# Optimization experiments

Hardware: AMD Instinct MI355X
Metric: run time of the kernel (lower is better)

The kernel has to match this reference:

```python
import jax, jax.numpy as jnp
import numpy as np

D_MODEL = 768
D_STATE = 128
D_CONV = 4
EXPAND = 4
D_INNER = EXPAND * D_MODEL  # 3072
DT_RANK = 48  # ceil(768/16), mamba default dt_rank='auto'
H_MLP = 768
EPS = 1e-6


def setup_inputs() -> dict:
    key = jax.random.key(0)
    ks = jax.random.split(key, 12)
    B, T = 1, 384

    def rn(k, shape, s=0.02):
        return jax.random.normal(k, shape, jnp.float32) * s

    inp = {}
    inp["x"] = jax.random.normal(ks[0], (B, 3 * T, D_MODEL), jnp.float32)
    inp["ln_w"] = jnp.ones((6, D_MODEL), jnp.float32)  # ln1..ln6 RMSNorm weights
    # 3 independent Mamba blocks, params stacked on leading dim
    inp["in_proj_w"] = rn(ks[1], (3, 2 * D_INNER, D_MODEL))
    inp["conv_w"] = rn(ks[2], (3, D_INNER, 1, D_CONV), 0.1)  # depthwise causal conv1d
    inp["conv_b"] = rn(ks[3], (3, D_INNER), 0.1)
    inp["x_proj_w"] = rn(ks[4], (3, DT_RANK + 2 * D_STATE, D_INNER))
    inp["dt_proj_w"] = rn(ks[5], (3, D_INNER, DT_RANK), 0.1)
    inp["dt_proj_b"] = rn(ks[6], (3, D_INNER), 0.1) - 4.0  # small dt after softplus
    A = jnp.tile(jnp.arange(1, D_STATE + 1, dtype=jnp.float32)[None, None, :], (3, D_INNER, 1))
    inp["A_log"] = jnp.log(A)  # mamba S4D-real init
    inp["D_skip"] = jnp.ones((3, D_INNER), jnp.float32)
    inp["out_proj_w"] = rn(ks[7], (3, D_MODEL, D_INNER))
    # 3 GatedMLPs: fc1 -> 2*hidden (value, gate), silu gate, fc2 -> out
    inp["fc1_w"] = rn(ks[8], (3, 2 * H_MLP, D_MODEL))
    inp["fc1_b"] = jnp.zeros((3, 2 * H_MLP), jnp.float32)
    inp["fc2_w"] = rn(ks[9], (3, D_MODEL, H_MLP))
    inp["fc2_b"] = jnp.zeros((3, D_MODEL), jnp.float32)
    return inp


def _rmsnorm(x, w):
    v = jnp.mean(jnp.square(x), axis=-1, keepdims=True)
    return x * jax.lax.rsqrt(v + EPS) * w


def _mamba(u, in_w, cw, cb, xp_w, dt_w, dt_b, A_log, D_skip, out_w):
    # u: (B, T, D_MODEL)
    Bsz = u.shape[0]
    xz = u @ in_w.T  # (B,T,2*Di)
    x, z = jnp.split(xz, 2, axis=-1)
    # causal depthwise conv1d over time
    xc = jax.lax.conv_general_dilated(
        jnp.swapaxes(x, 1, 2), cw, (1,), [(D_CONV - 1, 0)],
        feature_group_count=D_INNER)  # (B,Di,T)
    x = jax.nn.silu(jnp.swapaxes(xc, 1, 2) + cb)  # (B,T,Di)
    x_dbl = x @ xp_w.T  # (B,T,dt_rank+2N)
    dt = x_dbl[..., :DT_RANK]
    Bm = x_dbl[..., DT_RANK:DT_RANK + D_STATE]
    Cm = x_dbl[..., DT_RANK + D_STATE:]
    delta = jax.nn.softplus(dt @ dt_w.T + dt_b)  # (B,T,Di)
    A = -jnp.exp(A_log)  # (Di,N)

    def step(h, inp):
        d_t, B_t, C_t, u_t = inp  # (B,Di),(B,N),(B,N),(B,Di)
        h = jnp.exp(d_t[:, :, None] * A) * h + (d_t * u_t)[:, :, None] * B_t[:, None, :]
        y = jnp.einsum('bdn,bn->bd', h, C_t)
        return h, y

    h0 = jnp.zeros((Bsz, D_INNER, D_STATE), u.dtype)
    xs = tuple(jnp.swapaxes(a, 0, 1) for a in (delta, Bm, Cm, x))  # time-major
    _, ys = jax.lax.scan(jax.checkpoint(step), h0, xs)
    y = jnp.swapaxes(ys, 0, 1) + x * D_skip  # (B,T,Di)
    return (y * jax.nn.silu(z)) @ out_w.T  # (B,T,D_MODEL)


def _gmlp(x, w1, b1, w2, b2):
    h = x @ w1.T + b1
    a, g = jnp.split(h, 2, axis=-1)
    return (jax.nn.silu(g) * a) @ w2.T + b2


def reference(x, ln_w, in_proj_w, conv_w, conv_b, x_proj_w, dt_proj_w, dt_proj_b,
              A_log, D_skip, out_proj_w, fc1_w, fc1_b, fc2_w, fc2_b):
    t = x.shape[1] // 3
    outs = []
    for i in range(3):  # music / up / down branches
        b = x[:, i * t:(i + 1) * t]
        b = b + _mamba(_rmsnorm(b, ln_w[2 * i]), in_proj_w[i], conv_w[i], conv_b[i],
                       x_proj_w[i], dt_proj_w[i], dt_proj_b[i], A_log[i], D_skip[i],
                       out_proj_w[i])
        b = b + _gmlp(_rmsnorm(b, ln_w[2 * i + 1]), fc1_w[i], fc1_b[i], fc2_w[i], fc2_b[i])
        outs.append(b)
    return jnp.concatenate(outs, axis=1)
```

## Files before the change

kernel.cpp:

```cpp
#include <hip/hip_runtime.h>
#include <hip/hip_bf16.h>

#define TSEQ 384
#define DMODEL 768
#define DINNER 3072
#define DSTATE 128
#define DTRANK 48
#define XPROJ_N (DTRANK + 2*DSTATE)
#define NSEG 3
#define LOG2E 1.44269504088896340736f
#define LN2F  0.69314718055994530942f

typedef __attribute__((ext_vector_type(8))) short short8;
typedef __attribute__((ext_vector_type(4))) float floatx4;
typedef unsigned short u16;
typedef unsigned int u32;

__device__ __forceinline__ float bf2f(u16 u) {
    return __uint_as_float(((unsigned)u) << 16);
}
__device__ __forceinline__ float ldf(const void* p, size_t i, int bf) {
    return bf ? bf2f(((const u16*)p)[i]) : ((const float*)p)[i];
}
__device__ __forceinline__ void stf(void* p, size_t i, float v, int bf) {
    if (bf) ((__hip_bfloat16*)p)[i] = __float2bfloat16(v);
    else    ((float*)p)[i] = v;
}
__device__ __forceinline__ float silu_f(float v) { return v / (1.f + __expf(-v)); }
__device__ __forceinline__ u16 f2bf(float f) {
    unsigned u = __float_as_uint(f);
    return (u16)((u + 0x7FFFu + ((u >> 16) & 1u)) >> 16);
}

__device__ __forceinline__ float exp2_fast(float x) {
#if __has_builtin(__builtin_amdgcn_exp2f)
    return __builtin_amdgcn_exp2f(x);
#else
    return exp2f(x);
#endif
}

template<int CTRL>
__device__ __forceinline__ float ror_add(float x) {
    int r = __builtin_amdgcn_update_dpp(0, __float_as_int(x), CTRL, 0xF, 0xF, true);
    return x + __int_as_float(r);
}

__device__ __forceinline__ void gl16(const void* g, void* l) {
    __builtin_amdgcn_global_load_lds(
        (const __attribute__((address_space(1))) u32*)g,
        (__attribute__((address_space(3))) u32*)l, 16, 0, 0);
}

__global__ void k_detect(const unsigned* lnw_bits, int* flag) {
    if (threadIdx.x == 0) {
        flag[0] = (lnw_bits[0] == 0x3F803F80u) ? 1 : 0;
    }
}

__global__ __launch_bounds__(256) void k_rmsnorm(
    const void* src, int src_is_f32, const void* lnw, int wbase,
    u16* out, const int* flagp)
{
    int bf  = *flagp;
    int sbf = src_is_f32 ? 0 : bf;
    int r   = blockIdx.x;
    int seg = r / TSEQ;
    int wrow = 2*seg + wbase;
    int tid = threadIdx.x;
    float v[3]; float s = 0.f;
    #pragma unroll
    for (int j = 0; j < 3; ++j) {
        int e = j*256 + tid;
        v[j] = ldf(src, (size_t)r*DMODEL + e, sbf);
        s += v[j]*v[j];
    }
    __shared__ float red[256];
    red[tid] = s; __syncthreads();
    for (int st = 128; st > 0; st >>= 1) {
        if (tid < st) red[tid] += red[tid+st];
        __syncthreads();
    }
    float rs = rsqrtf(red[0]/(float)DMODEL + 1e-6f);
    #pragma unroll
    for (int j = 0; j < 3; ++j) {
        int e = j*256 + tid;
        out[(size_t)r*DMODEL + e] = f2bf(v[j]*rs*ldf(lnw, (size_t)wrow*DMODEL + e, bf));
    }
}

__global__ __launch_bounds__(256) void k_gemm(
    const float* A, const void* W, const void* bias,
    float* C, const int* flagp, int M, int N, int K, int lda)
{
    int bf  = *flagp;
    int seg = blockIdx.z;
    int mbase = blockIdx.y * 64, nbase = blockIdx.x * 64;
    int tid = threadIdx.x;
    int tx = tid & 15, ty = tid >> 4;

    __shared__ float As[16][68];
    __shared__ float Ws[16][68];

    const float* Ag = A + (size_t)seg*M*lda;
    size_t segW = (size_t)seg*N*K;

    int lrow = tid >> 2;
    int lk   = (tid & 3) * 4;
    int wn   = nbase + lrow;

    float acc[4][4];
    #pragma unroll
    for (int i = 0; i < 4; ++i)
        #pragma unroll
        for (int j = 0; j < 4; ++j) acc[i][j] = 0.f;

    for (int kt = 0; kt < K; kt += 16) {
        float4 av = *reinterpret_cast<const float4*>(Ag + (size_t)(mbase+lrow)*lda + kt + lk);
        As[lk+0][lrow] = av.x; As[lk+1][lrow] = av.y;
        As[lk+2][lrow] = av.z; As[lk+3][lrow] = av.w;
        float w0=0.f, w1=0.f, w2=0.f, w3=0.f;
        if (wn < N) {
            size_t off = segW + (size_t)wn*K + kt + lk;
            if (bf) {
                ushort4 q = *reinterpret_cast<const ushort4*>((const u16*)W + off);
                w0 = bf2f(q.x); w1 = bf2f(q.y); w2 = bf2f(q.z); w3 = bf2f(q.w);
            } else {
                float4 f = *reinterpret_cast<const float4*>((const float*)W + off);
                w0 = f.x; w1 = f.y; w2 = f.z; w3 = f.w;
            }
        }
        Ws[lk+0][lrow] = w0; Ws[lk+1][lrow] = w1;
        Ws[lk+2][lrow] = w2; Ws[lk+3][lrow] = w3;
        __syncthreads();
        #pragma unroll
        for (int kk = 0; kk < 16; ++kk) {
            float4 a4 = *reinterpret_cast<const float4*>(&As[kk][ty*4]);
            float4 b4 = *reinterpret_cast<const float4*>(&Ws[kk][tx*4]);
            float ar[4] = {a4.x, a4.y, a4.z, a4.w};
            float br[4] = {b4.x, b4.y, b4.z, b4.w};
            #pragma unroll
            for (int i = 0; i < 4; ++i)
                #pragma unroll
                for (int j = 0; j < 4; ++j)
                    acc[i][j] = fmaf(ar[i], br[j], acc[i][j]);
        }
        __syncthreads();
    }

    #pragma unroll
    for (int i = 0; i < 4; ++i) {
        int m = mbase + ty*4 + i;
        #pragma unroll
        for (int j = 0; j < 4; ++j) {
            int n = nbase + tx*4 + j;
            if (n < N) {
                float v = acc[i][j] + ldf(bias, (size_t)seg*N + n, bf);
                v = (v > 20.f) ? v : log1pf(__expf(v));
                C[((size_t)(seg*M + m))*N + n] = v;
            }
        }
    }
}

__global__ __launch_bounds__(256) void k_gemm_mfma64g(
    const u16* A, const void* W, const void* bias, const void* resid,
    int resid_flagged, void* C, int c_mode, const int* flagp,
    int M, int N, int K)
{
    int bf  = *flagp;
    int seg = blockIdx.z;
    int mbase = blockIdx.y * 64, nbase = blockIdx.x * 64;
    int tid = threadIdx.x;
    int w = tid >> 6, lane = tid & 63;
    int wm = w >> 1, wn = w & 1;
    int quad = lane >> 4, l16 = lane & 15;

    __shared__ short As[3][64*64];
    __shared__ short Ws[3][64*64];

    const u16* Ag = A + (size_t)seg*M*K + (size_t)mbase*K;
    size_t segWK = (size_t)seg*N*K;
    int nk = K >> 6;

    int srow = lane >> 3;
    int scol = ((lane & 7) ^ srow) * 8;
    int swz  = (l16 & 7) * 8;

    floatx4 acc[2][2];
    #pragma unroll
    for (int i = 0; i < 2; ++i)
        #pragma unroll
        for (int j = 0; j < 2; ++j)
            acc[i][j] = (floatx4){0.f, 0.f, 0.f, 0.f};

    auto CMP = [&](int b) {
        #pragma unroll
        for (int kk = 0; kk < 2; ++kk) {
            short8 af[2], bfr[2];
            #pragma unroll
            for (int i = 0; i < 2; ++i) {
                int row = wm*32 + i*16 + l16;
                af[i] = *reinterpret_cast<const short8*>(
                    &As[b][row*64 + (((kk*4 + quad)*8) ^ swz)]);
            }
            #pragma unroll
            for (int j = 0; j < 2; ++j) {
                int row = wn*32 + j*16 + l16;
                bfr[j] = *reinterpret_cast<const short8*>(
                    &Ws[b][row*64 + (((kk*4 + quad)*8) ^ swz)]);
            }
            #pragma unroll
            for (int i = 0; i < 2; ++i)
                #pragma unroll
                for (int j = 0; j < 2; ++j)
                    acc[i][j] = __builtin_amdgcn_mfma_f32_16x16x32_bf16(af[i], bfr[j], acc[i][j], 0, 0, 0);
        }
    };

    if (bf) {
        const u16* Wb = (const u16*)W;
        auto STG = [&](int t, int b) {
            size_t kt = (size_t)t << 6;
            #pragma unroll
            for (int i8 = 0; i8 < 2; ++i8) {
                int rbase = w*16 + i8*8;
                gl16(Ag + (size_t)(rbase + srow)*K + kt + scol, &As[b][rbase*64]);
                int wr = nbase + rbase + srow;
                if (wr > N - 1) wr = N - 1;
                gl16(Wb + segWK + (size_t)wr*K + kt + scol, &Ws[b][rbase*64]);
            }
        };
        STG(0, 0);
        STG(1, 1);
        for (int t = 0; t < nk - 2; ++t) {
            STG(t + 2, (t + 2) % 3);
            asm volatile("s_waitcnt vmcnt(8)" ::: "memory");
            __builtin_amdgcn_s_barrier();
            __builtin_amdgcn_sched_barrier(0);
            CMP(t % 3);
            asm volatile("" ::: "memory");
            __builtin_amdgcn_s_barrier();
        }
        asm volatile("s_waitcnt vmcnt(4)" ::: "memory");
        __builtin_amdgcn_s_barrier();
        __builtin_amdgcn_sched_barrier(0);
        CMP((nk - 2) % 3);
        asm volatile("" ::: "memory");
        __builtin_amdgcn_s_barrier();
        asm volatile("s_waitcnt vmcnt(0)" ::: "memory");
        __builtin_amdgcn_s_barrier();
        __builtin_amdgcn_sched_barrier(0);
        CMP((nk - 1) % 3);
    } else {
        const float* Wf = (const float*)W + segWK;
        int row2 = tid >> 2;
        int wr2 = nbase + row2; if (wr2 > N - 1) wr2 = N - 1;
        for (int t = 0; t < nk; ++t) {
            size_t kt = (size_t)t << 6;
            #pragma unroll
            for (int i8 = 0; i8 < 2; ++i8) {
                int rbase = w*16 + i8*8;
                gl16(Ag + (size_t)(rbase + srow)*K + kt + scol, &As[0][rbase*64]);
            }
            const float* wp = Wf + (size_t)wr2*K + kt;
            #pragma unroll
            for (int h2 = 0; h2 < 2; ++h2) {
                int gs = (tid & 3) + h2*4;
                short8 s;
                #pragma unroll
                for (int q2 = 0; q2 < 8; ++q2) s[q2] = (short)f2bf(wp[gs*8 + q2]);
                *reinterpret_cast<short8*>(&Ws[0][row2*64 + ((gs ^ (row2 & 7)) * 8)]) = s;
            }
            __syncthreads();
            CMP(0);
            __syncthreads();
        }
    }

    #pragma unroll
    for (int i = 0; i < 2; ++i) {
        #pragma unroll
        for (int reg = 0; reg < 4; ++reg) {
            int grow = mbase + wm*32 + i*16 + quad*4 + reg;
            #pragma unroll
            for (int j = 0; j < 2; ++j) {
                int gcol = nbase + wn*32 + j*16 + l16;
                if (gcol < N) {
                    float v = acc[i][j][reg];
                    if (bias) v += ldf(bias, (size_t)seg*N + gcol, bf);
                    size_t idx = ((size_t)(seg*M + grow))*N + gcol;
                    if (resid) v += resid_flagged ? ldf(resid, idx, bf)
                                                  : ((const float*)resid)[idx];
                    if      (c_mode == 0) ((float*)C)[idx] = v;
                    else if (c_mode == 1) ((u16*)C)[idx] = f2bf(v);
                    else                  stf(C, idx, v, bf);
                }
            }
        }
    }
}

__global__ __launch_bounds__(256) void k_fc1_gate_g(
    const u16* A, const void* W, const void* bias, u16* act, const int* flagp)
{
    const int M = TSEQ, K = DMODEL, NF = 2*DMODEL;
    int bf  = *flagp;
    int seg = blockIdx.z;
    int mbase = blockIdx.y * 64, nbase = blockIdx.x * 64;
    int tid = threadIdx.x;
    int w = tid >> 6, lane = tid & 63;
    int wm = w >> 1, wn = w & 1;
    int quad = lane >> 4, l16 = lane & 15;

    __shared__ short As[2][64*64];
    __shared__ short Wa[2][64*64];
    __shared__ short Wg[2][64*64];

    const u16* Ag  = A + (size_t)seg*M*K + (size_t)mbase*K;
    const u16* Wap = (const u16*)W + (size_t)seg*NF*K + (size_t)nbase*K;
    const u16* Wgp = Wap + (size_t)DMODEL*K;
    int nk = K >> 6;

    int srow = lane >> 3;
    int scol = ((lane & 7) ^ srow) * 8;
    int swz  = (l16 & 7) * 8;

    floatx4 acca[2][2], accg[2][2];
    #pragma unroll
    for (int i = 0; i < 2; ++i)
        #pragma unroll
        for (int j = 0; j < 2; ++j) {
            acca[i][j] = (floatx4){0.f, 0.f, 0.f, 0.f};
            accg[i][j] = (floatx4){0.f, 0.f, 0.f, 0.f};
        }

    auto CMP = [&](int b) {
        #pragma unroll
        for (int kk = 0; kk < 2; ++kk) {
            short8 af[2], ba[2], bg[2];
            #pragma unroll
            for (int i = 0; i < 2; ++i) {
                int row = wm*32 + i*16 + l16;
                af[i] = *reinterpret_cast<const short8*>(
                    &As[b][row*64 + (((kk*4 + quad)*8) ^ swz)]);
            }
            #pragma unroll
            for (int j = 0; j < 2; ++j) {
                int row = wn*32 + j*16 + l16;
                int col = ((kk*4 + quad)*8) ^ swz;
                ba[j] = *reinterpret_cast<const short8*>(&Wa[b][row*64 + col]);
                bg[j] = *reinterpret_cast<const short8*>(&Wg[b][row*64 + col]);
            }
            #pragma unroll
            for (int i = 0; i < 2; ++i)
                #pragma unroll
                for (int j = 0; j < 2; ++j) {
                    acca[i][j] = __builtin_amdgcn_mfma_f32_16x16x32_bf16(af[i], ba[j], acca[i][j], 0, 0, 0);
                    accg[i][j] = __builtin_amdgcn_mfma_f32_16x16x32_bf16(af[i], bg[j], accg[i][j], 0, 0, 0);
                }
        }
    };

    if (bf) {
        auto STG = [&](int t, int b) {
            size_t kt = (size_t)t << 6;
            #pragma unroll
            for (int i8 = 0; i8 < 2; ++i8) {
                int rbase = w*16 + i8*8;
                size_t so = (size_t)(rbase + srow)*K + kt + scol;
                gl16(Ag  + so, &As[b][rbase*64]);
                gl16(Wap + so, &Wa[b][rbase*64]);
                gl16(Wgp + so, &Wg[b][rbase*64]);
            }
        };
        STG(0, 0);
        for (int t = 0; t < nk - 1; ++t) {
            STG(t + 1, (t + 1) & 1);
            asm volatile("s_waitcnt vmcnt(6)" ::: "memory");
            __builtin_amdgcn_s_barrier();
            __builtin_amdgcn_sched_barrier(0);
            CMP(t & 1);
            asm volatile("" ::: "memory");
            __builtin_amdgcn_s_barrier();
        }
        asm volatile("s_waitcnt vmcnt(0)" ::: "memory");
        __builtin_amdgcn_s_barrier();
        __builtin_amdgcn_sched_barrier(0);
        CMP((nk - 1) & 1);
    } else {
        const float* Waf = (const float*)W + (size_t)seg*NF*K + (size_t)nbase*K;
        const float* Wgf = Waf + (size_t)DMODEL*K;
        int row2 = tid >> 2;
        for (int t = 0; t < nk; ++t) {
            size_t kt = (size_t)t << 6;
            #pragma unroll
            for (int i8 = 0; i8 < 2; ++i8) {
                int rbase = w*16 + i8*8;
                gl16(Ag + (size_t)(rbase + srow)*K + kt + scol, &As[0][rbase*64]);
            }
            #pragma unroll
            for (int h2 = 0; h2 < 2; ++h2) {
                int gs = (tid & 3) + h2*4;
                int wcol = (gs ^ (row2 & 7)) * 8;
                short8 sa, sg;
                const float* wpa = Waf + (size_t)row2*K + kt + gs*8;
                const float* wpg = Wgf + (size_t)row2*K + kt + gs*8;
                #pragma unroll
                for (int q2 = 0; q2 < 8; ++q2) { sa[q2] = (short)f2bf(wpa[q2]); sg[q2] = (short)f2bf(wpg[q2]); }
                *reinterpret_cast<short8*>(&Wa[0][row2*64 + wcol]) = sa;
                *reinterpret_cast<short8*>(&Wg[0][row2*64 + wcol]) = sg;
            }
            __syncthreads();
            CMP(0);
            __syncthreads();
        }
    }

    #pragma unroll
    for (int i = 0; i < 2; ++i) {
        #pragma unroll
        for (int reg = 0; reg < 4; ++reg) {
            int grow = mbase + wm*32 + i*16 + quad*4 + reg;
            #pragma unroll
            for (int j = 0; j < 2; ++j) {
                int gcol = nbase + wn*32 + j*16 + l16;
                float va = acca[i][j][reg] + ldf(bias, (size_t)seg*NF + gcol, bf);
                float vg = accg[i][j][reg] + ldf(bias, (size_t)seg*NF + DMODEL + gcol, bf);
                act[((size_t)(seg*M + grow))*DMODEL + gcol] = f2bf(va * silu_f(vg));
            }
        }
    }
}

__global__ __launch_bounds__(256) void k_conv(
    const u16* xz, const void* cw, const void* cb, u16* xconv, const int* flagp)
{
    int bf = *flagp;
    size_t gid = (size_t)blockIdx.x*256 + threadIdx.x;
    int d = (int)(gid % DINNER);
    size_t rt = gid / DINNER;
    int t = (int)(rt % TSEQ);
    int seg = (int)(rt / TSEQ);
    float acc = ldf(cb, (size_t)seg*DINNER + d, bf);
    const u16* xs = xz + (size_t)seg*TSEQ*(2*DINNER);
    #pragma unroll
    for (int j = 0; j < 4; ++j) {
        int ts = t - 3 + j;
        if (ts >= 0)
            acc = fmaf(ldf(cw, ((size_t)seg*DINNER + d)*4 + j, bf),
                       bf2f(xs[(size_t)ts*(2*DINNER) + d]), acc);
    }
    xconv[gid] = f2bf(silu_f(acc));
}

#define WSCH 4
#define WSCT 8
#define NPAIR (TSEQ/(2*WSCT))
#define NBX   (DINNER/WSCH)
#define GUARD_TH 0.04f

__global__ __launch_bounds__(64) void k_scan_wave(
    const float* delta, const u16* xconv, const float* xdbl, const u16* xz,
    const void* A_log, const void* D_skip, u16* yout, const int* flagp)
{
    int bf   = flagp[0];
    int seg  = blockIdx.y;
    int bx = (int)blockIdx.x;
    bx = (bx & 7) * (NBX/8) + (bx >> 3);
    int dbase = bx * WSCH;
    int lane = threadIdx.x;
    int ch = lane >> 4, sl = lane & 15;
    int d = dbase + ch;

    __shared__ float4 BUF[2][WSCT][64];
    __shared__ float  DLB2[WSCT][8];

    float a[8];
    size_t abase = ((size_t)seg*DINNER + d)*DSTATE + (size_t)sl*8;
    #pragma unroll
    for (int j = 0; j < 8; ++j)
        a[j] = -__expf(ldf(A_log, abase + j, bf)) * LOG2E;
    float gl[8]; float gmax = 0.f;
    gl[0] = 0.f;
    #pragma unroll
    for (int j = 1; j < 8; ++j) {
        gl[j] = (a[j] - a[j-1]) * LN2F;
        gmax = fmaxf(gmax, fabsf(gl[j]));
    }
    float wg = gmax;
    #pragma unroll
    for (int k = 32; k >= 1; k >>= 1) wg = fmaxf(wg, __shfl_xor(wg, k));
    float a0  = a[0];
    float Dsk = ldf(D_skip, (size_t)seg*DINNER + d, bf);
    float dskg = (sl == 0) ? Dsk : 0.f;

    const float* xdbl_s = xdbl + (size_t)seg*TSEQ*XPROJ_N;
    int loff = DTRANK + (lane & 15)*8 + ((lane >> 4) & 1)*4 + ((lane >> 5) ? DSTATE : 0);
    const float* srcl = xdbl_s + loff;

    const float* delta_s = delta + (size_t)seg*TSEQ*DINNER + dbase;
    const u16*   xconv_s = xconv + (size_t)seg*TSEQ*DINNER + dbase;
    const u16*   z_s     = xz    + (size_t)seg*TSEQ*(2*DINNER) + DINNER + dbase + ch;
    u16*         y_s     = yout  + (size_t)seg*TSEQ*DINNER + dbase + ch;

    float4  pdel = (float4){0.f, 0.f, 0.f, 0.f};
    ushort4 pu   = (ushort4){0, 0, 0, 0};
    u16     pz   = 0;

    auto STAGE = [&](int tile, int buf) {
        const float* rb = srcl + (size_t)tile*WSCT*XPROJ_N;
        #pragma unroll
        for (int t = 0; t < WSCT; ++t)
            gl16(rb + (size_t)t*XPROJ_N, &BUF[buf][t][0]);
    };
    auto PLOAD = [&](int tile) {
        if (lane < WSCT) {
            size_t ro = (size_t)(tile*WSCT + lane)*DINNER;
            pdel = *reinterpret_cast<const float4*>(delta_s + ro);
            pu   = *reinterpret_cast<const ushort4*>(xconv_s + ro);
        }
    };
    auto DSTORE = [&]() -> bool {
        if (lane < WSCT) {
            float4 w0 = (float4){pdel.x, bf2f(pu.x), pdel.y, bf2f(pu.y)};
            float4 w1 = (float4){pdel.z, bf2f(pu.z), pdel.w, bf2f(pu.w)};
            *reinterpret_cast<float4*>(&DLB2[lane][0]) = w0;
            *reinterpret_cast<float4*>(&DLB2[lane][4]) = w1;
        }
        float m4 = fmaxf(fmaxf(pdel.x, pdel.y), fmaxf(pdel.z, pdel.w));
        return __any(m4 * wg > GUARD_TH);
    };

    float h[8];
    #pragma unroll
    for (int j = 0; j < 8; ++j) h[j] = 0.f;
    float yr = 0.f;

    float2 duA, duB, duC;
    float4 b0A, b1A, c0A, c1A;
    float4 b0B, b1B, c0B, c1B;
    float4 b0C, b1C, c0C, c1C;

#define LOADOPS(BP, T, S) do {                                                \
    du##S = *reinterpret_cast<const float2*>(&DLB2[T][ch*2]);                 \
    b0##S = (BP)[(T)*64 + sl];                                                \
    b1##S = (BP)[(T)*64 + 16 + sl];                                           \
    c0##S = (BP)[(T)*64 + 32 + sl];                                           \
    c1##S = (BP)[(T)*64 + 48 + sl];                                           \
} while (0)

#define COMPUTE(S, T) do {                                                    \
    float del = du##S.x, ut = du##S.y;                                        \
    float duu = del * ut;                                                     \
    float e0,e1,e2,e3,e4,e5,e6,e7;                                            \
    if (gf) {                                                                 \
        e0 = exp2_fast(del * a0);                                             \
        e1 = e0 * fmaf(del, gl[1], 1.f);                                      \
        e2 = e1 * fmaf(del, gl[2], 1.f);                                      \
        e3 = e2 * fmaf(del, gl[3], 1.f);                                      \
        e4 = e3 * fmaf(del, gl[4], 1.f);                                      \
        e5 = e4 * fmaf(del, gl[5], 1.f);                                      \
        e6 = e5 * fmaf(del, gl[6], 1.f);                                      \
        e7 = e6 * fmaf(del, gl[7], 1.f);                                      \
    } else {                                                                  \
        e0 = exp2_fast(del*a[0]); e1 = exp2_fast(del*a[1]);                   \
        e2 = exp2_fast(del*a[2]); e3 = exp2_fast(del*a[3]);                   \
        e4 = exp2_fast(del*a[4]); e5 = exp2_fast(del*a[5]);                   \
        e6 = exp2_fast(del*a[6]); e7 = exp2_fast(del*a[7]);                   \
    }                                                                         \
    h[0] = fmaf(e0, h[0], duu*b0##S.x);                                       \
    h[1] = fmaf(e1, h[1], duu*b0##S.y);                                       \
    h[2] = fmaf(e2, h[2], duu*b0##S.z);                                       \
    h[3] = fmaf(e3, h[3], duu*b0##S.w);                                       \
    h[4] = fmaf(e4, h[4], duu*b1##S.x);                                       \
    h[5] = fmaf(e5, h[5], duu*b1##S.y);                                       \
    h[6] = fmaf(e6, h[6], duu*b1##S.z);                                       \
    h[7] = fmaf(e7, h[7], duu*b1##S.w);                                       \
    float p0 = ut * dskg;                                                     \
    p0 = fmaf(h[0], c0##S.x, p0);                                             \
    p0 = fmaf(h[1], c0##S.y, p0);                                             \
    p0 = fmaf(h[2], c0##S.z, p0);                                             \
    p0 = fmaf(h[3], c0##S.w, p0);                                             \
    float p1 = h[4]*c1##S.x;                                                  \
    p1 = fmaf(h[5], c1##S.y, p1);                                             \
    p1 = fmaf(h[6], c1##S.z, p1);                                             \
    p1 = fmaf(h[7], c1##S.w, p1);                                             \
    float p = p0 + p1;                                                        \
    p = ror_add<0x128>(p);                                                    \
    p = ror_add<0x124>(p);                                                    \
    p = ror_add<0x122>(p);                                                    \
    p = ror_add<0x121>(p);                                                    \
    if (sl == (half8 | (T))) yr = p;                                          \
} while (0)

    auto do_tile = [&](const float4* bp, bool gf, int half8) {
        LOADOPS(bp, 0, A);
        LOADOPS(bp, 1, B);
        LOADOPS(bp, 2, C);
        COMPUTE(A, 0);
        LOADOPS(bp, 3, A);
        COMPUTE(B, 1);
        LOADOPS(bp, 4, B);
        COMPUTE(C, 2);
        LOADOPS(bp, 5, C);
        COMPUTE(A, 3);
        LOADOPS(bp, 6, A);
        COMPUTE(B, 4);
        LOADOPS(bp, 7, B);
        COMPUTE(C, 5);
        COMPUTE(A, 6);
        COMPUTE(B, 7);
    };

    STAGE(0, 0);
    PLOAD(0);

    for (int p = 0; p < NPAIR; ++p) {
        int tA = 2*p;
        asm volatile("s_waitcnt vmcnt(0)" ::: "memory");
        bool exA = DSTORE();
        STAGE(tA + 1, 1);
        PLOAD(tA + 1);
        pz = z_s[(size_t)(p*16 + sl) * (size_t)(2*DINNER)];
        __builtin_amdgcn_sched_barrier(0);
        do_tile(&BUF[0][0][0], !exA, 0);
        asm volatile("s_waitcnt vmcnt(0)" ::: "memory");
        bool exB = DSTORE();
        if (tA + 2 < 2*NPAIR) {
            STAGE(tA + 2, 0);
            PLOAD(tA + 2);
        }
        __builtin_amdgcn_sched_barrier(0);
        do_tile(&BUF[1][0][0], !exB, 8);
        y_s[(size_t)(p*16 + sl) * (size_t)DINNER] = f2bf(yr * silu_f(bf2f(pz)));
        yr = 0.f;
    }
#undef LOADOPS
#undef COMPUTE
}

extern "C" void kernel_launch(void* const* d_in, const int* in_sizes, int n_in,
                              void* d_out, int out_size, void* d_ws, size_t ws_size,
                              hipStream_t stream) {
    const void* x     = d_in[0];
    const void* lnw   = d_in[1];
    const void* inw   = d_in[2];
    const void* convw = d_in[3];
    const void* convb = d_in[4];
    const void* xpw   = d_in[5];
    const void* dtw   = d_in[6];
    const void* dtb   = d_in[7];
    const void* alog  = d_in[8];
    const void* dsk   = d_in[9];
    const void* outw  = d_in[10];
    const void* fc1w  = d_in[11];
    const void* fc1b  = d_in[12];
    const void* fc2w  = d_in[13];
    const void* fc2b  = d_in[14];

    int* flag = (int*)d_ws;
    char* wsb = (char*)d_ws;
    const size_t N_U    = (size_t)NSEG*TSEQ*DMODEL;
    const size_t N_XZ   = (size_t)NSEG*TSEQ*2*DINNER;
    const size_t N_XC   = (size_t)NSEG*TSEQ*DINNER;
    const size_t N_XDBL = (size_t)NSEG*TSEQ*XPROJ_N;

    u16*   u     = (u16*)(wsb + 16);
    u16*   xz    = u + N_U;
    u16*   xconv = xz + N_XZ;
    float* xdbl  = (float*)(xconv + N_XC);
    float* delta = xdbl + N_XDBL;
    u16*   yfin  = (u16*)(delta + N_XC);
    float* b1    = (float*)(yfin + N_XC);
    u16*   actb  = (u16*)(b1 + N_U);

    k_detect<<<1, 64, 0, stream>>>((const unsigned*)lnw, flag);

    k_rmsnorm<<<NSEG*TSEQ, 256, 0, stream>>>(x, 0, lnw, 0, u, flag);
    k_gemm_mfma64g<<<dim3(96, 6, NSEG), 256, 0, stream>>>(u, inw, nullptr, nullptr, 0,
        xz, 1, flag, TSEQ, 2*DINNER, DMODEL);
    k_conv<<<(NSEG*TSEQ*DINNER)/256, 256, 0, stream>>>(xz, convw, convb, xconv, flag);
    k_gemm_mfma64g<<<dim3(5, 6, NSEG), 256, 0, stream>>>(xconv, xpw, nullptr, nullptr, 0,
        xdbl, 0, flag, TSEQ, XPROJ_N, DINNER);
    k_gemm<<<dim3(48, 6, NSEG), 256, 0, stream>>>(xdbl, dtw, dtb,
        delta, flag, TSEQ, DINNER, DTRANK, XPROJ_N);

    k_scan_wave<<<dim3(NBX, NSEG), 64, 0, stream>>>(
        delta, xconv, xdbl, xz, alog, dsk, yfin, flag);

    k_gemm_mfma64g<<<dim3(12, 6, NSEG), 256, 0, stream>>>(yfin, outw, nullptr, x, 1,
        b1, 0, flag, TSEQ, DMODEL, DINNER);

    k_rmsnorm<<<NSEG*TSEQ, 256, 0, stream>>>(b1, 1, lnw, 1, u, flag);
    k_fc1_gate_g<<<dim3(12, 6, NSEG), 256, 0, stream>>>(u, fc1w, fc1b, actb, flag);
    k_gemm_mfma64g<<<dim3(12, 6, NSEG), 256, 0, stream>>>(actb, fc2w, fc2b, b1, 0,
        d_out, 2, flag, TSEQ, DMODEL, DMODEL);
}
```

Measured before the change: 540.1 us.

## Split-K the x_proj and out_proj GEMMs with atomic accumulation; shorten scan exp chain

Adds a split-K mode to the MFMA GEMM kernel. The x_proj and out_proj GEMMs (K=3072) each run as four K-slices that atomically add fp32 partial sums into zeroed outputs, with bias and residual added by slice 0 only. This targets the low block counts of those GEMMs (90 and 216 blocks) by raising parallelism, at the cost of two memsets and atomic traffic. The scan also computes four exps instead of one and replaces the long serial multiply chain of decay factors with shorter ones, and it rebalances the C-dot reduction tree to cut dependency depth.

```diff
diff --git a/kernel.cpp b/kernel.cpp
--- a/kernel.cpp
+++ b/kernel.cpp
@@ -166,10 +166,11 @@
 __global__ __launch_bounds__(256) void k_gemm_mfma64g(
     const u16* A, const void* W, const void* bias, const void* resid,
     int resid_flagged, void* C, int c_mode, const int* flagp,
-    int M, int N, int K)
+    int M, int N, int K, int ksplit)
 {
     int bf  = *flagp;
-    int seg = blockIdx.z;
+    int zz  = blockIdx.z;
+    int seg = zz / ksplit, ks = zz - seg*ksplit;
     int mbase = blockIdx.y * 64, nbase = blockIdx.x * 64;
     int tid = threadIdx.x;
     int w = tid >> 6, lane = tid & 63;
@@ -179,9 +180,10 @@
     __shared__ short As[3][64*64];
     __shared__ short Ws[3][64*64];
 
-    const u16* Ag = A + (size_t)seg*M*K + (size_t)mbase*K;
+    int nk = (K >> 6) / ksplit;
+    size_t k0 = ((size_t)ks * nk) << 6;
+    const u16* Ag = A + (size_t)seg*M*K + (size_t)mbase*K + k0;
     size_t segWK = (size_t)seg*N*K;
-    int nk = K >> 6;
 
     int srow = lane >> 3;
     int scol = ((lane & 7) ^ srow) * 8;
@@ -228,7 +230,7 @@
                 gl16(Ag + (size_t)(rbase + srow)*K + kt + scol, &As[b][rbase*64]);
                 int wr = nbase + rbase + srow;
                 if (wr > N - 1) wr = N - 1;
-                gl16(Wb + segWK + (size_t)wr*K + kt + scol, &Ws[b][rbase*64]);
+                gl16(Wb + segWK + (size_t)wr*K + k0 + kt + scol, &Ws[b][rbase*64]);
             }
         };
         STG(0, 0);
@@ -263,7 +265,7 @@
                 int rbase = w*16 + i8*8;
                 gl16(Ag + (size_t)(rbase + srow)*K + kt + scol, &As[0][rbase*64]);
             }
-            const float* wp = Wf + (size_t)wr2*K + kt;
+            const float* wp = Wf + (size_t)wr2*K + k0 + kt;
             #pragma unroll
             for (int h2 = 0; h2 < 2; ++h2) {
                 int gs = (tid & 3) + h2*4;
@@ -288,13 +290,22 @@
                 int gcol = nbase + wn*32 + j*16 + l16;
                 if (gcol < N) {
                     float v = acc[i][j][reg];
-                    if (bias) v += ldf(bias, (size_t)seg*N + gcol, bf);
                     size_t idx = ((size_t)(seg*M + grow))*N + gcol;
-                    if (resid) v += resid_flagged ? ldf(resid, idx, bf)
-                                                  : ((const float*)resid)[idx];
-                    if      (c_mode == 0) ((float*)C)[idx] = v;
-                    else if (c_mode == 1) ((u16*)C)[idx] = f2bf(v);
-                    else                  stf(C, idx, v, bf);
+                    if (ksplit == 1) {
+                        if (bias) v += ldf(bias, (size_t)seg*N + gcol, bf);
+                        if (resid) v += resid_flagged ? ldf(resid, idx, bf)
+                                                      : ((const float*)resid)[idx];
+                        if      (c_mode == 0) ((float*)C)[idx] = v;
+                        else if (c_mode == 1) ((u16*)C)[idx] = f2bf(v);
+                        else                  stf(C, idx, v, bf);
+                    } else {
+                        if (ks == 0) {
+                            if (bias)  v += ldf(bias, (size_t)seg*N + gcol, bf);
+                            if (resid) v += resid_flagged ? ldf(resid, idx, bf)
+                                                          : ((const float*)resid)[idx];
+                        }
+                        atomicAdd(&((float*)C)[idx], v);
+                    }
                 }
             }
         }
@@ -481,17 +492,16 @@
     #pragma unroll
     for (int j = 0; j < 8; ++j)
         a[j] = -__expf(ldf(A_log, abase + j, bf)) * LOG2E;
-    float gl[8]; float gmax = 0.f;
+    float gl[8];
     gl[0] = 0.f;
     #pragma unroll
-    for (int j = 1; j < 8; ++j) {
+    for (int j = 1; j < 8; ++j)
         gl[j] = (a[j] - a[j-1]) * LN2F;
-        gmax = fmaxf(gmax, fabsf(gl[j]));
-    }
+    float gmax = fmaxf(fmaxf(fabsf(gl[1]), fabsf(gl[3])),
+                       fmaxf(fabsf(gl[5]), fabsf(gl[7])));
     float wg = gmax;
     #pragma unroll
     for (int k = 32; k >= 1; k >>= 1) wg = fmaxf(wg, __shfl_xor(wg, k));
-    float a0  = a[0];
     float Dsk = ldf(D_skip, (size_t)seg*DINNER + d, bf);
     float dskg = (sl == 0) ? Dsk : 0.f;
 
@@ -555,13 +565,13 @@
     float duu = del * ut;                                                     \
     float e0,e1,e2,e3,e4,e5,e6,e7;                                            \
     if (gf) {                                                                 \
-        e0 = exp2_fast(del * a0);                                             \
+        e0 = exp2_fast(del*a[0]);                                             \
+        e2 = exp2_fast(del*a[2]);                                             \
+        e4 = exp2_fast(del*a[4]);                                             \
+        e6 = exp2_fast(del*a[6]);                                             \
         e1 = e0 * fmaf(del, gl[1], 1.f);                                      \
-        e2 = e1 * fmaf(del, gl[2], 1.f);                                      \
         e3 = e2 * fmaf(del, gl[3], 1.f);                                      \
-        e4 = e3 * fmaf(del, gl[4], 1.f);                                      \
         e5 = e4 * fmaf(del, gl[5], 1.f);                                      \
-        e6 = e5 * fmaf(del, gl[6], 1.f);                                      \
         e7 = e6 * fmaf(del, gl[7], 1.f);                                      \
     } else {                                                                  \
         e0 = exp2_fast(del*a[0]); e1 = exp2_fast(del*a[1]);                   \
@@ -577,16 +587,12 @@
     h[5] = fmaf(e5, h[5], duu*b1##S.y);                                       \
     h[6] = fmaf(e6, h[6], duu*b1##S.z);                                       \
     h[7] = fmaf(e7, h[7], duu*b1##S.w);                                       \
-    float p0 = ut * dskg;                                                     \
-    p0 = fmaf(h[0], c0##S.x, p0);                                             \
-    p0 = fmaf(h[1], c0##S.y, p0);                                             \
-    p0 = fmaf(h[2], c0##S.z, p0);                                             \
-    p0 = fmaf(h[3], c0##S.w, p0);                                             \
-    float p1 = h[4]*c1##S.x;                                                  \
-    p1 = fmaf(h[5], c1##S.y, p1);                                             \
-    p1 = fmaf(h[6], c1##S.z, p1);                                             \
-    p1 = fmaf(h[7], c1##S.w, p1);                                             \
-    float p = p0 + p1;                                                        \
+    float q0 = fmaf(h[0], c0##S.x, ut*dskg);                                  \
+    q0 = fmaf(h[1], c0##S.y, q0);                                             \
+    float q1 = h[2]*c0##S.z;  q1 = fmaf(h[3], c0##S.w, q1);                   \
+    float q2 = h[4]*c1##S.x;  q2 = fmaf(h[5], c1##S.y, q2);                   \
+    float q3 = h[6]*c1##S.z;  q3 = fmaf(h[7], c1##S.w, q3);                   \
+    float p = (q0 + q1) + (q2 + q3);                                          \
     p = ror_add<0x128>(p);                                                    \
     p = ror_add<0x124>(p);                                                    \
     p = ror_add<0x122>(p);                                                    \
@@ -676,24 +682,26 @@
     u16*   actb  = (u16*)(b1 + N_U);
 
     k_detect<<<1, 64, 0, stream>>>((const unsigned*)lnw, flag);
+    hipMemsetAsync(xdbl, 0, N_XDBL*sizeof(float), stream);
+    hipMemsetAsync(b1,   0, N_U*sizeof(float),   stream);
 
     k_rmsnorm<<<NSEG*TSEQ, 256, 0, stream>>>(x, 0, lnw, 0, u, flag);
     k_gemm_mfma64g<<<dim3(96, 6, NSEG), 256, 0, stream>>>(u, inw, nullptr, nullptr, 0,
-        xz, 1, flag, TSEQ, 2*DINNER, DMODEL);
+        xz, 1, flag, TSEQ, 2*DINNER, DMODEL, 1);
     k_conv<<<(NSEG*TSEQ*DINNER)/256, 256, 0, stream>>>(xz, convw, convb, xconv, flag);
-    k_gemm_mfma64g<<<dim3(5, 6, NSEG), 256, 0, stream>>>(xconv, xpw, nullptr, nullptr, 0,
-        xdbl, 0, flag, TSEQ, XPROJ_N, DINNER);
+    k_gemm_mfma64g<<<dim3(5, 6, NSEG*4), 256, 0, stream>>>(xconv, xpw, nullptr, nullptr, 0,
+        xdbl, 0, flag, TSEQ, XPROJ_N, DINNER, 4);
     k_gemm<<<dim3(48, 6, NSEG), 256, 0, stream>>>(xdbl, dtw, dtb,
         delta, flag, TSEQ, DINNER, DTRANK, XPROJ_N);
 
     k_scan_wave<<<dim3(NBX, NSEG), 64, 0, stream>>>(
         delta, xconv, xdbl, xz, alog, dsk, yfin, flag);
 
-    k_gemm_mfma64g<<<dim3(12, 6, NSEG), 256, 0, stream>>>(yfin, outw, nullptr, x, 1,
-        b1, 0, flag, TSEQ, DMODEL, DINNER);
+    k_gemm_mfma64g<<<dim3(12, 6, NSEG*4), 256, 0, stream>>>(yfin, outw, nullptr, x, 1,
+        b1, 0, flag, TSEQ, DMODEL, DINNER, 4);
 
     k_rmsnorm<<<NSEG*TSEQ, 256, 0, stream>>>(b1, 1, lnw, 1, u, flag);
     k_fc1_gate_g<<<dim3(12, 6, NSEG), 256, 0, stream>>>(u, fc1w, fc1b, actb, flag);
     k_gemm_mfma64g<<<dim3(12, 6, NSEG), 256, 0, stream>>>(actb, fc2w, fc2b, b1, 0,
-        d_out, 2, flag, TSEQ, DMODEL, DMODEL);
-}
+        d_out, 2, flag, TSEQ, DMODEL, DMODEL, 1);
+}
```

New measurement: 512.3 us. 1.05x faster.
